# Kernel optimization log

Measured on AMD Instinct MI355X. Metric: run time of the kernel, lower is better.

The kernel has to match this reference:

```python
import jax, jax.numpy as jnp
import numpy as np

B, T, C = 4, 2048, 1024
H, DH = 16, 64  # num_heads, head_size; H*DH == C


def setup_inputs() -> dict:
    key = jax.random.key(0)
    ks = jax.random.split(key, 6)
    s = C ** -0.5  # mimic nn.Linear default init scale roughly
    x = jax.random.normal(ks[0], (B, T, C), dtype=jnp.float32)
    Wq = jax.random.normal(ks[1], (H, C, DH), dtype=jnp.float32) * s
    Wk = jax.random.normal(ks[2], (H, C, DH), dtype=jnp.float32) * s
    Wv = jax.random.normal(ks[3], (H, C, DH), dtype=jnp.float32) * s
    Wo = jax.random.normal(ks[4], (C, C), dtype=jnp.float32) * s
    bo = jax.random.normal(ks[5], (C,), dtype=jnp.float32) * s
    return {"x": x, "Wq": Wq, "Wk": Wk, "Wv": Wv, "Wo": Wo, "bo": bo}


def reference(x, Wq, Wk, Wv, Wo, bo):
    # per-head projections (no bias, as in nanoGPT Head)
    q = jnp.einsum('btc,hcd->bhtd', x, Wq)
    k = jnp.einsum('btc,hcd->bhtd', x, Wk)
    v = jnp.einsum('btc,hcd->bhtd', x, Wv)
    scale = DH ** -0.5
    scores = jnp.einsum('bhtd,bhsd->bhts', q, k) * scale  # [B,H,T,T]
    causal = jnp.tril(jnp.ones((T, T), dtype=bool))
    scores = jnp.where(causal, scores, jnp.float32(-jnp.inf))
    attn = jax.nn.softmax(scores, axis=-1)
    out = jnp.einsum('bhts,bhsd->bhtd', attn, v)  # [B,H,T,DH]
    out = out.transpose(0, 2, 1, 3).reshape(B, T, C)  # concat heads
    return out @ Wo.T + bo  # output projection (dropout=0.0 -> identity)
```

## Files before the change

kernel.cpp:

```cpp
#include <hip/hip_runtime.h>
#include <hip/hip_bf16.h>

constexpr int kB = 4, kT = 2048, kC = 1024, kH = 16, kD = 64;

typedef __attribute__((ext_vector_type(8))) short bf16x8;
typedef __attribute__((ext_vector_type(4))) short bf16x4;
typedef __attribute__((ext_vector_type(4))) float f32x4;
typedef unsigned short u16;

__device__ inline u16 f2b(float f) {
    __bf16 h = (__bf16)f;
    return __builtin_bit_cast(u16, h);
}

__device__ __forceinline__ void gl_lds16(const u16* g, u16* l) {
    __builtin_amdgcn_global_load_lds(
        (__attribute__((address_space(1))) const void*)g,
        (__attribute__((address_space(3))) void*)l, 16, 0, 0);
}

__global__ __launch_bounds__(256) void prep_kernel(const float* __restrict__ xf,
                                                   u16* __restrict__ xb,
                                                   const float* __restrict__ Wq,
                                                   const float* __restrict__ Wk,
                                                   const float* __restrict__ Wv,
                                                   u16* __restrict__ Wt) {
    __shared__ u16 tile[64][66];
    if (blockIdx.x < 8192) {
        int i = (blockIdx.x * 256 + threadIdx.x) * 4;
        float4 v = *(const float4*)(xf + i);
        ushort4 o;
        o.x = f2b(v.x); o.y = f2b(v.y); o.z = f2b(v.z); o.w = f2b(v.w);
        *(ushort4*)(xb + i) = o;
        return;
    }
    int blk = blockIdx.x - 8192;
    int ct = blk & 15;
    int h  = (blk >> 4) & 15;
    int which = blk >> 8;
    const float* W = (which == 0) ? Wq : (which == 1) ? Wk : Wv;
    const float* src = W + ((size_t)h * kC + ct * 64) * kD;
    int tid = threadIdx.x;
    int dr = (tid & 15) * 4;
    int cr = tid >> 4;
    #pragma unroll
    for (int pass = 0; pass < 4; pass++) {
        int c = pass * 16 + cr;
        float4 v = *(const float4*)(src + (size_t)c * kD + dr);
        tile[c][dr + 0] = f2b(v.x);
        tile[c][dr + 1] = f2b(v.y);
        tile[c][dr + 2] = f2b(v.z);
        tile[c][dr + 3] = f2b(v.w);
    }
    __syncthreads();
    u16* dst = Wt + ((size_t)(which * kH + h) * kD) * kC + ct * 64;
    int c4 = (tid & 15) * 4;
    int d0 = tid >> 4;
    #pragma unroll
    for (int pass = 0; pass < 4; pass++) {
        int d = pass * 16 + d0;
        ushort4 pk;
        pk.x = tile[c4 + 0][d];
        pk.y = tile[c4 + 1][d];
        pk.z = tile[c4 + 2][d];
        pk.w = tile[c4 + 3][d];
        *(ushort4*)(dst + (size_t)d * kC + c4) = pk;
    }
}

__global__ __launch_bounds__(256) void qkv_kernel(const u16* __restrict__ x,
                                                  const u16* __restrict__ Wt,
                                                  u16* __restrict__ q,
                                                  u16* __restrict__ k,
                                                  u16* __restrict__ vT) {
    __shared__ u16 Ash[128 * 32];
    __shared__ u16 Bsh[128 * 32];
    const int tid = threadIdx.x;
    const int lane = tid & 63;
    const int w = tid >> 6;
    const int mblk = blockIdx.x & 63;
    const int nblk = blockIdx.x >> 6;
    const int m0 = mblk * 128, n0 = nblk * 128;
    const int wm = (w >> 1) * 64, wn = (w & 1) * 64;
    const int col = lane & 15, quad = lane >> 4;

    const int rowa = tid >> 2;
    const int kc = (tid & 3) * 8;
    const u16* gA = x + (size_t)(m0 + rowa) * kC + kc;
    const u16* gB = Wt + (size_t)(n0 + rowa) * kC + kc;
    u16* lA = Ash + tid * 8;
    u16* lB = Bsh + tid * 8;

    f32x4 z = {0.f, 0.f, 0.f, 0.f};
    f32x4 acc[4][4];
    #pragma unroll
    for (int mi = 0; mi < 4; mi++)
        #pragma unroll
        for (int ni = 0; ni < 4; ni++) acc[mi][ni] = z;

    for (int k0 = 0; k0 < kC; k0 += 32) {
        __syncthreads();
        gl_lds16(gA + k0, lA);
        gl_lds16(gA + (size_t)64 * kC + k0, lA + 64 * 32);
        gl_lds16(gB + k0, lB);
        gl_lds16(gB + (size_t)64 * kC + k0, lB + 64 * 32);
        __syncthreads();
        bf16x8 a[4], b[4];
        #pragma unroll
        for (int mi = 0; mi < 4; mi++)
            a[mi] = *(const bf16x8*)&Ash[(wm + mi * 16 + col) * 32 + quad * 8];
        #pragma unroll
        for (int ni = 0; ni < 4; ni++)
            b[ni] = *(const bf16x8*)&Bsh[(wn + ni * 16 + col) * 32 + quad * 8];
        #pragma unroll
        for (int mi = 0; mi < 4; mi++)
            #pragma unroll
            for (int ni = 0; ni < 4; ni++)
                acc[mi][ni] = __builtin_amdgcn_mfma_f32_16x16x32_bf16(a[mi], b[ni], acc[mi][ni], 0, 0, 0);
    }

    const int nq = n0 + wn;
    const int which = nq >> 10;
    const int h = (nq & 1023) >> 6;
    const int mq = m0 + wm;
    const int b_ = mq >> 11;
    const int tq = mq & 2047;
    if (which < 2) {
        const float qs = (which == 0) ? 0.1803368801111204f : 1.0f;
        u16* base = ((which == 0) ? q : k) + ((size_t)(b_ * kH + h) * kT) * kD;
        #pragma unroll
        for (int mi = 0; mi < 4; mi++)
            #pragma unroll
            for (int ni = 0; ni < 4; ni++)
                #pragma unroll
                for (int r = 0; r < 4; r++) {
                    int t = tq + mi * 16 + quad * 4 + r;
                    base[(size_t)t * kD + ni * 16 + col] = f2b(acc[mi][ni][r] * qs);
                }
    } else {
        u16* base = vT + ((size_t)(b_ * kH + h) * kD) * kT;
        #pragma unroll
        for (int mi = 0; mi < 4; mi++)
            #pragma unroll
            for (int ni = 0; ni < 4; ni++) {
                int d = ni * 16 + col;
                int t = tq + mi * 16 + quad * 4;
                ushort4 pk;
                pk.x = f2b(acc[mi][ni][0]);
                pk.y = f2b(acc[mi][ni][1]);
                pk.z = f2b(acc[mi][ni][2]);
                pk.w = f2b(acc[mi][ni][3]);
                *(ushort4*)(base + (size_t)d * kT + t) = pk;
            }
    }
}

__device__ __forceinline__ void attn_step(const bf16x8 (&ka)[2][2],
                                          const bf16x4 (&va)[2][4],
                                          const bf16x8 (&qa)[2][2],
                                          f32x4 (&o)[2][4],
                                          float (&l_)[2],
                                          bool needmask,
                                          int s0, int t0, int col, int quad) {
    f32x4 z = {0.f, 0.f, 0.f, 0.f};
    f32x4 st[2][2];
    #pragma unroll
    for (int si = 0; si < 2; si++)
        #pragma unroll
        for (int mi = 0; mi < 2; mi++) {
            f32x4 a = __builtin_amdgcn_mfma_f32_16x16x32_bf16(ka[si][0], qa[mi][0], z, 0, 0, 0);
            st[si][mi] = __builtin_amdgcn_mfma_f32_16x16x32_bf16(ka[si][1], qa[mi][1], a, 0, 0, 0);
        }
    bf16x4 pb[2][2];
    #pragma unroll
    for (int mi = 0; mi < 2; mi++)
        #pragma unroll
        for (int si = 0; si < 2; si++) {
            bf16x4 pk;
            #pragma unroll
            for (int r = 0; r < 4; r++) {
                float p = __builtin_amdgcn_exp2f(st[si][mi][r]);
                if (needmask) {
                    int sg = s0 + si * 16 + quad * 4 + r;
                    int tg = t0 + mi * 16 + col;
                    if (sg > tg) p = 0.f;
                }
                l_[mi] += p;
                pk[r] = (short)f2b(p);
            }
            pb[mi][si] = pk;
        }
    #pragma unroll
    for (int si = 0; si < 2; si++)
        #pragma unroll
        for (int dt = 0; dt < 4; dt++)
            #pragma unroll
            for (int mi = 0; mi < 2; mi++)
                o[mi][dt] = __builtin_amdgcn_mfma_f32_16x16x16bf16_1k(va[si][dt], pb[mi][si], o[mi][dt], 0, 0, 0);
}

__global__ __launch_bounds__(256) void attn_kernel(const u16* __restrict__ q,
                                                   const u16* __restrict__ kmat,
                                                   const u16* __restrict__ vT,
                                                   u16* __restrict__ att,
                                                   const float* __restrict__ Wo,
                                                   u16* __restrict__ Wob) {
    __shared__ u16 Ksh[3][2048];
    __shared__ u16 Vsh[3][2048];
    if (blockIdx.x >= 512) {
        int i = ((blockIdx.x - 512) * 256 + threadIdx.x) * 4;
        float4 v = *(const float4*)(Wo + i);
        ushort4 o;
        o.x = f2b(v.x); o.y = f2b(v.y); o.z = f2b(v.z); o.w = f2b(v.w);
        *(ushort4*)(Wob + i) = o;
        return;
    }
    const int tid = threadIdx.x;
    const int lane = tid & 63;
    const int w = tid >> 6;
    const int bh = blockIdx.x & 63;
    const int p8 = blockIdx.x >> 6;
    const int p = p8 * 4 + w;
    const int t0a = p * 32;
    const int t0b = (63 - p) * 32;
    const int L = 63 - p8 * 4;
    const int col = lane & 15, quad = lane >> 4;

    const u16* qbase = q + (size_t)bh * kT * kD;
    const u16* kbase = kmat + (size_t)bh * kT * kD;
    const u16* vbase = vT + (size_t)bh * kD * kT;

    const int krow = tid >> 3, kpos = tid & 7;
    const u16* gK = kbase + (size_t)krow * kD + ((kpos ^ (krow & 7)) * 8);
    const int vrow = tid >> 2, vpos = tid & 3;
    const u16* gV = vbase + (size_t)vrow * kT + ((vpos ^ ((vrow >> 1) & 3)) * 8);

    bf16x8 qa[2][2][2];
    #pragma unroll
    for (int tile = 0; tile < 2; tile++) {
        int t0 = tile ? t0b : t0a;
        #pragma unroll
        for (int mi = 0; mi < 2; mi++)
            #pragma unroll
            for (int c2 = 0; c2 < 2; c2++)
                qa[tile][mi][c2] = *(const bf16x8*)(qbase + (size_t)(t0 + mi * 16 + col) * kD + c2 * 32 + quad * 8);
    }

    f32x4 z = {0.f, 0.f, 0.f, 0.f};
    f32x4 oA[2][4], oB[2][4];
    #pragma unroll
    for (int mi = 0; mi < 2; mi++)
        #pragma unroll
        for (int dt = 0; dt < 4; dt++) { oA[mi][dt] = z; oB[mi][dt] = z; }
    float lA[2] = {0.f, 0.f}, lB[2] = {0.f, 0.f};

    auto stage = [&](int buf, int tile) {
        gl_lds16(gK + (size_t)(tile * 32) * kD, &Ksh[buf][tid * 8]);
        gl_lds16(gV + tile * 32, &Vsh[buf][tid * 8]);
    };

    auto body = [&](int tile, int buf) {
        const int s0 = tile * 32;
        bf16x8 ka[2][2];
        #pragma unroll
        for (int si = 0; si < 2; si++) {
            int row = si * 16 + col;
            #pragma unroll
            for (int c2 = 0; c2 < 2; c2++)
                ka[si][c2] = *(const bf16x8*)&Ksh[buf][row * 64 + (((c2 * 4 + quad) ^ (row & 7)) * 8)];
        }
        bf16x4 va[2][4];
        #pragma unroll
        for (int si = 0; si < 2; si++)
            #pragma unroll
            for (int dt = 0; dt < 4; dt++) {
                int row = dt * 16 + col;
                int sb = si * 2 + (quad >> 1);
                va[si][dt] = *(const bf16x4*)&Vsh[buf][row * 32 + ((sb ^ ((row >> 1) & 3)) * 8) + (quad & 1) * 4];
            }
        if (s0 <= t0b)
            attn_step(ka, va, qa[1], oB, lB, s0 == t0b, s0, t0b, col, quad);
        if (s0 <= t0a)
            attn_step(ka, va, qa[0], oA, lA, s0 == t0a, s0, t0a, col, quad);
    };

    stage(0, 0);
    if (L >= 1) stage(1, 1);
    int i = 0;
    for (; i + 2 <= L; i++) {
        asm volatile("s_barrier" ::: "memory");
        stage((i + 2) % 3, i + 2);
        asm volatile("s_waitcnt vmcnt(4)" ::: "memory");
        body(i, i % 3);
    }
    if (L >= 1) {
        asm volatile("s_barrier" ::: "memory");
        asm volatile("s_waitcnt vmcnt(2)" ::: "memory");
        body(L - 1, (L - 1) % 3);
    }
    asm volatile("s_barrier" ::: "memory");
    asm volatile("s_waitcnt vmcnt(0)" ::: "memory");
    body(L, L % 3);

    #pragma unroll
    for (int mi = 0; mi < 2; mi++) {
        lA[mi] += __shfl_xor(lA[mi], 16, 64);
        lA[mi] += __shfl_xor(lA[mi], 32, 64);
        lB[mi] += __shfl_xor(lB[mi], 16, 64);
        lB[mi] += __shfl_xor(lB[mi], 32, 64);
    }

    const int b = bh / kH, hh = bh % kH;
    #pragma unroll
    for (int tile = 0; tile < 2; tile++) {
        int t0 = tile ? t0b : t0a;
        #pragma unroll
        for (int mi = 0; mi < 2; mi++) {
            float inv = 1.0f / (tile ? lB[mi] : lA[mi]);
            int t = t0 + mi * 16 + col;
            #pragma unroll
            for (int dt = 0; dt < 4; dt++) {
                f32x4 s = tile ? oB[mi][dt] : oA[mi][dt];
                ushort4 pk;
                pk.x = f2b(s[0] * inv);
                pk.y = f2b(s[1] * inv);
                pk.z = f2b(s[2] * inv);
                pk.w = f2b(s[3] * inv);
                *(ushort4*)(att + ((size_t)b * kT + t) * kC + hh * kD + dt * 16 + quad * 4) = pk;
            }
        }
    }
}

__global__ __launch_bounds__(256) void oproj_kernel(const u16* __restrict__ att,
                                                    const u16* __restrict__ Wo,
                                                    const float* __restrict__ bo,
                                                    float* __restrict__ out) {
    __shared__ u16 Ash[128 * 32];
    __shared__ u16 Bsh[128 * 32];
    const int tid = threadIdx.x;
    const int lane = tid & 63;
    const int w = tid >> 6;
    const int mblk = blockIdx.x & 63;
    const int nblk = blockIdx.x >> 6;
    const int m0 = mblk * 128, n0 = nblk * 128;
    const int wm = (w >> 1) * 64, wn = (w & 1) * 64;
    const int col = lane & 15, quad = lane >> 4;

    const int rowa = tid >> 2;
    const int kc = (tid & 3) * 8;
    const u16* gA = att + (size_t)(m0 + rowa) * kC + kc;
    const u16* gB = Wo + (size_t)(n0 + rowa) * kC + kc;
    u16* lA = Ash + tid * 8;
    u16* lB = Bsh + tid * 8;

    f32x4 z = {0.f, 0.f, 0.f, 0.f};
    f32x4 acc[4][4];
    #pragma unroll
    for (int mi = 0; mi < 4; mi++)
        #pragma unroll
        for (int ni = 0; ni < 4; ni++) acc[mi][ni] = z;

    for (int k0 = 0; k0 < kC; k0 += 32) {
        __syncthreads();
        gl_lds16(gA + k0, lA);
        gl_lds16(gA + (size_t)64 * kC + k0, lA + 64 * 32);
        gl_lds16(gB + k0, lB);
        gl_lds16(gB + (size_t)64 * kC + k0, lB + 64 * 32);
        __syncthreads();
        bf16x8 a[4], b[4];
        #pragma unroll
        for (int mi = 0; mi < 4; mi++)
            a[mi] = *(const bf16x8*)&Ash[(wm + mi * 16 + col) * 32 + quad * 8];
        #pragma unroll
        for (int ni = 0; ni < 4; ni++)
            b[ni] = *(const bf16x8*)&Bsh[(wn + ni * 16 + col) * 32 + quad * 8];
        #pragma unroll
        for (int mi = 0; mi < 4; mi++)
            #pragma unroll
            for (int ni = 0; ni < 4; ni++)
                acc[mi][ni] = __builtin_amdgcn_mfma_f32_16x16x32_bf16(a[mi], b[ni], acc[mi][ni], 0, 0, 0);
    }

    float bias[4];
    #pragma unroll
    for (int ni = 0; ni < 4; ni++) bias[ni] = bo[n0 + wn + ni * 16 + col];

    #pragma unroll
    for (int mi = 0; mi < 4; mi++)
        #pragma unroll
        for (int ni = 0; ni < 4; ni++)
            #pragma unroll
            for (int r = 0; r < 4; r++) {
                int m = m0 + wm + mi * 16 + quad * 4 + r;
                out[(size_t)m * kC + n0 + wn + ni * 16 + col] = acc[mi][ni][r] + bias[ni];
            }
}

extern "C" void kernel_launch(void* const* d_in, const int* in_sizes, int n_in,
                              void* d_out, int out_size, void* d_ws, size_t ws_size,
                              hipStream_t stream) {
    const float* x  = (const float*)d_in[0];
    const float* Wq = (const float*)d_in[1];
    const float* Wk = (const float*)d_in[2];
    const float* Wv = (const float*)d_in[3];
    const float* Wo = (const float*)d_in[4];
    const float* bo = (const float*)d_in[5];
    float* out = (float*)d_out;

    char* ws = (char*)d_ws;
    u16* Wt  = (u16*)ws;
    u16* xb  = Wt + (size_t)3 * kH * kD * kC;
    u16* qb  = xb + (size_t)kB * kT * kC;
    u16* kb  = qb + (size_t)kB * kH * kT * kD;
    u16* vTb = kb + (size_t)kB * kH * kT * kD;
    u16* att = xb;
    u16* Wob = Wt;

    prep_kernel<<<dim3(8192 + 768), dim3(256), 0, stream>>>(x, xb, Wq, Wk, Wv, Wt);
    qkv_kernel<<<dim3(1536), dim3(256), 0, stream>>>(xb, Wt, qb, kb, vTb);
    attn_kernel<<<dim3(512 + 1024), dim3(256), 0, stream>>>(qb, kb, vTb, att, Wo, Wob);
    oproj_kernel<<<dim3(512), dim3(256), 0, stream>>>(att, Wob, bo, out);
}
```

Measured before the change: 254.1 us.

## Split attention KV loop across two wave groups with LDS reduction

Doubles the attention block to 512 threads. Each half of the block processes half of the key/value tiles for the same query rows, using its own triple-buffered LDS staging area. The partial outputs and row sums are then combined through an LDS scratch reduction before normalization and store. The aim is to shorten the serial KV loop per block and raise occupancy and parallelism. The cost is extra LDS traffic, more barriers, and a larger shared-memory footprint per block.

```diff
diff --git a/kernel.cpp b/kernel.cpp
--- a/kernel.cpp
+++ b/kernel.cpp
@@ -199,16 +199,15 @@
                 o[mi][dt] = __builtin_amdgcn_mfma_f32_16x16x16bf16_1k(va[si][dt], pb[mi][si], o[mi][dt], 0, 0, 0);
 }
 
-__global__ __launch_bounds__(256) void attn_kernel(const u16* __restrict__ q,
+__global__ __launch_bounds__(512) void attn_kernel(const u16* __restrict__ q,
                                                    const u16* __restrict__ kmat,
                                                    const u16* __restrict__ vT,
                                                    u16* __restrict__ att,
                                                    const float* __restrict__ Wo,
                                                    u16* __restrict__ Wob) {
-    __shared__ u16 Ksh[3][2048];
-    __shared__ u16 Vsh[3][2048];
+    __shared__ u16 shmem[24576];
     if (blockIdx.x >= 512) {
-        int i = ((blockIdx.x - 512) * 256 + threadIdx.x) * 4;
+        int i = ((blockIdx.x - 512) * 512 + threadIdx.x) * 4;
         float4 v = *(const float4*)(Wo + i);
         ushort4 o;
         o.x = f2b(v.x); o.y = f2b(v.y); o.z = f2b(v.z); o.w = f2b(v.w);
@@ -218,22 +217,28 @@
     const int tid = threadIdx.x;
     const int lane = tid & 63;
     const int w = tid >> 6;
+    const int half = w >> 2;
     const int bh = blockIdx.x & 63;
     const int p8 = blockIdx.x >> 6;
-    const int p = p8 * 4 + w;
+    const int p = p8 * 4 + (w & 3);
     const int t0a = p * 32;
     const int t0b = (63 - p) * 32;
     const int L = 63 - p8 * 4;
+    const int n = (L + 1) / 2;
+    const int tb = half ? n : 0;
     const int col = lane & 15, quad = lane >> 4;
 
     const u16* qbase = q + (size_t)bh * kT * kD;
     const u16* kbase = kmat + (size_t)bh * kT * kD;
     const u16* vbase = vT + (size_t)bh * kD * kT;
 
-    const int krow = tid >> 3, kpos = tid & 7;
+    const int tl = tid & 255;
+    const int krow = tl >> 3, kpos = tl & 7;
     const u16* gK = kbase + (size_t)krow * kD + ((kpos ^ (krow & 7)) * 8);
-    const int vrow = tid >> 2, vpos = tid & 3;
+    const int vrow = tl >> 2, vpos = tl & 3;
     const u16* gV = vbase + (size_t)vrow * kT + ((vpos ^ ((vrow >> 1) & 3)) * 8);
+    u16* Kb0 = shmem + half * 12288;
+    u16* Vb0 = Kb0 + 6144;
 
     bf16x8 qa[2][2][2];
     #pragma unroll
@@ -255,19 +260,21 @@
     float lA[2] = {0.f, 0.f}, lB[2] = {0.f, 0.f};
 
     auto stage = [&](int buf, int tile) {
-        gl_lds16(gK + (size_t)(tile * 32) * kD, &Ksh[buf][tid * 8]);
-        gl_lds16(gV + tile * 32, &Vsh[buf][tid * 8]);
+        gl_lds16(gK + (size_t)(tile * 32) * kD, Kb0 + buf * 2048 + tl * 8);
+        gl_lds16(gV + tile * 32, Vb0 + buf * 2048 + tl * 8);
     };
 
     auto body = [&](int tile, int buf) {
         const int s0 = tile * 32;
+        const u16* Kb = Kb0 + buf * 2048;
+        const u16* Vb = Vb0 + buf * 2048;
         bf16x8 ka[2][2];
         #pragma unroll
         for (int si = 0; si < 2; si++) {
             int row = si * 16 + col;
             #pragma unroll
             for (int c2 = 0; c2 < 2; c2++)
-                ka[si][c2] = *(const bf16x8*)&Ksh[buf][row * 64 + (((c2 * 4 + quad) ^ (row & 7)) * 8)];
+                ka[si][c2] = *(const bf16x8*)&Kb[row * 64 + (((c2 * 4 + quad) ^ (row & 7)) * 8)];
         }
         bf16x4 va[2][4];
         #pragma unroll
@@ -276,7 +283,7 @@
             for (int dt = 0; dt < 4; dt++) {
                 int row = dt * 16 + col;
                 int sb = si * 2 + (quad >> 1);
-                va[si][dt] = *(const bf16x4*)&Vsh[buf][row * 32 + ((sb ^ ((row >> 1) & 3)) * 8) + (quad & 1) * 4];
+                va[si][dt] = *(const bf16x4*)&Vb[row * 32 + ((sb ^ ((row >> 1) & 3)) * 8) + (quad & 1) * 4];
             }
         if (s0 <= t0b)
             attn_step(ka, va, qa[1], oB, lB, s0 == t0b, s0, t0b, col, quad);
@@ -284,23 +291,20 @@
             attn_step(ka, va, qa[0], oA, lA, s0 == t0a, s0, t0a, col, quad);
     };
 
-    stage(0, 0);
-    if (L >= 1) stage(1, 1);
-    int i = 0;
-    for (; i + 2 <= L; i++) {
+    stage(0, tb + 0);
+    stage(1, tb + 1);
+    for (int j = 0; j + 2 <= n - 1; j++) {
         asm volatile("s_barrier" ::: "memory");
-        stage((i + 2) % 3, i + 2);
+        stage((j + 2) % 3, tb + j + 2);
         asm volatile("s_waitcnt vmcnt(4)" ::: "memory");
-        body(i, i % 3);
-    }
-    if (L >= 1) {
-        asm volatile("s_barrier" ::: "memory");
-        asm volatile("s_waitcnt vmcnt(2)" ::: "memory");
-        body(L - 1, (L - 1) % 3);
-    }
+        body(tb + j, j % 3);
+    }
+    asm volatile("s_barrier" ::: "memory");
+    asm volatile("s_waitcnt vmcnt(2)" ::: "memory");
+    body(tb + n - 2, (n - 2) % 3);
     asm volatile("s_barrier" ::: "memory");
     asm volatile("s_waitcnt vmcnt(0)" ::: "memory");
-    body(L, L % 3);
+    body(tb + n - 1, (n - 1) % 3);
 
     #pragma unroll
     for (int mi = 0; mi < 2; mi++) {
@@ -310,22 +314,79 @@
         lB[mi] += __shfl_xor(lB[mi], 32, 64);
     }
 
+    float* scr = (float*)shmem;
+    const int slot = ((w & 3) * 64 + lane) * 35;
     const int b = bh / kH, hh = bh % kH;
-    #pragma unroll
-    for (int tile = 0; tile < 2; tile++) {
-        int t0 = tile ? t0b : t0a;
+
+    __syncthreads();
+    if (half == 1) {
+        #pragma unroll
+        for (int mi = 0; mi < 2; mi++)
+            #pragma unroll
+            for (int dt = 0; dt < 4; dt++)
+                #pragma unroll
+                for (int r = 0; r < 4; r++)
+                    scr[slot + (mi * 4 + dt) * 4 + r] = oA[mi][dt][r];
+        scr[slot + 32] = lA[0];
+        scr[slot + 33] = lA[1];
+    }
+    __syncthreads();
+    if (half == 0) {
         #pragma unroll
         for (int mi = 0; mi < 2; mi++) {
-            float inv = 1.0f / (tile ? lB[mi] : lA[mi]);
-            int t = t0 + mi * 16 + col;
+            #pragma unroll
+            for (int dt = 0; dt < 4; dt++)
+                #pragma unroll
+                for (int r = 0; r < 4; r++)
+                    oA[mi][dt][r] += scr[slot + (mi * 4 + dt) * 4 + r];
+            lA[mi] += scr[slot + 32 + mi];
+        }
+        #pragma unroll
+        for (int mi = 0; mi < 2; mi++) {
+            float inv = 1.0f / lA[mi];
+            int t = t0a + mi * 16 + col;
             #pragma unroll
             for (int dt = 0; dt < 4; dt++) {
-                f32x4 s = tile ? oB[mi][dt] : oA[mi][dt];
                 ushort4 pk;
-                pk.x = f2b(s[0] * inv);
-                pk.y = f2b(s[1] * inv);
-                pk.z = f2b(s[2] * inv);
-                pk.w = f2b(s[3] * inv);
+                pk.x = f2b(oA[mi][dt][0] * inv);
+                pk.y = f2b(oA[mi][dt][1] * inv);
+                pk.z = f2b(oA[mi][dt][2] * inv);
+                pk.w = f2b(oA[mi][dt][3] * inv);
+                *(ushort4*)(att + ((size_t)b * kT + t) * kC + hh * kD + dt * 16 + quad * 4) = pk;
+            }
+        }
+        #pragma unroll
+        for (int mi = 0; mi < 2; mi++)
+            #pragma unroll
+            for (int dt = 0; dt < 4; dt++)
+                #pragma unroll
+                for (int r = 0; r < 4; r++)
+                    scr[slot + (mi * 4 + dt) * 4 + r] = oB[mi][dt][r];
+        scr[slot + 32] = lB[0];
+        scr[slot + 33] = lB[1];
+    }
+    __syncthreads();
+    if (half == 1) {
+        #pragma unroll
+        for (int mi = 0; mi < 2; mi++) {
+            #pragma unroll
+            for (int dt = 0; dt < 4; dt++)
+                #pragma unroll
+                for (int r = 0; r < 4; r++)
+                    oB[mi][dt][r] += scr[slot + (mi * 4 + dt) * 4 + r];
+            lB[mi] += scr[slot + 32 + mi];
+        }
+        #pragma unroll
+        for (int mi = 0; mi < 2; mi++) {
+            float inv = 1.0f / lB[mi];
+            int t = t0b + mi * 16 + col;
+            #pragma unroll
+            for (int dt = 0; dt < 4; dt++) {
+                ushort4 pk;
+                pk.x = f2b(oB[mi][dt][0] * inv);
+                pk.y = f2b(oB[mi][dt][1] * inv);
+                pk.z = f2b(oB[mi][dt][2] * inv);
+                pk.w = f2b(oB[mi][dt][3] * inv);
                 *(ushort4*)(att + ((size_t)b * kT + t) * kC + hh * kD + dt * 16 + quad * 4) = pk;
             }
         }
@@ -419,6 +480,6 @@
 
     prep_kernel<<<dim3(8192 + 768), dim3(256), 0, stream>>>(x, xb, Wq, Wk, Wv, Wt);
     qkv_kernel<<<dim3(1536), dim3(256), 0, stream>>>(xb, Wt, qb, kb, vTb);
-    attn_kernel<<<dim3(512 + 1024), dim3(256), 0, stream>>>(qb, kb, vTb, att, Wo, Wob);
+    attn_kernel<<<dim3(512 + 512), dim3(512), 0, stream>>>(qb, kb, vTb, att, Wo, Wob);
     oproj_kernel<<<dim3(512), dim3(256), 0, stream>>>(att, Wob, bo, out);
 }
```

After: 254.7 us. No clear change (+0.2%).

## Give each wave private double-buffered K/V LDS staging and drop block barriers

Applied to the files above, without the earlier changes.

Replaces the block-shared triple-buffered K/V staging with per-wave double buffers, so each wave loads its own K/V tiles and iterates only up to its own causal limit. This removes the s_barrier calls and the extra tiles that shorter-range waves used to wait on. The cost is four times more global-to-LDS traffic for the same K/V tiles, since each wave loads them independently, plus a larger LDS footprint (64KB) that may lower occupancy.

```diff
diff --git a/kernel.cpp b/kernel.cpp
--- a/kernel.cpp
+++ b/kernel.cpp
@@ -205,8 +205,7 @@
                                                    u16* __restrict__ att,
                                                    const float* __restrict__ Wo,
                                                    u16* __restrict__ Wob) {
-    __shared__ u16 Ksh[3][2048];
-    __shared__ u16 Vsh[3][2048];
+    __shared__ u16 shmem[4][2][4096];
     if (blockIdx.x >= 512) {
         int i = ((blockIdx.x - 512) * 256 + threadIdx.x) * 4;
         float4 v = *(const float4*)(Wo + i);
@@ -223,17 +222,15 @@
     const int p = p8 * 4 + w;
     const int t0a = p * 32;
     const int t0b = (63 - p) * 32;
-    const int L = 63 - p8 * 4;
+    const int Lw = 63 - p8 * 4 - w;
     const int col = lane & 15, quad = lane >> 4;
 
     const u16* qbase = q + (size_t)bh * kT * kD;
     const u16* kbase = kmat + (size_t)bh * kT * kD;
     const u16* vbase = vT + (size_t)bh * kD * kT;
 
-    const int krow = tid >> 3, kpos = tid & 7;
-    const u16* gK = kbase + (size_t)krow * kD + ((kpos ^ (krow & 7)) * 8);
-    const int vrow = tid >> 2, vpos = tid & 3;
-    const u16* gV = vbase + (size_t)vrow * kT + ((vpos ^ ((vrow >> 1) & 3)) * 8);
+    const u16* gK0 = kbase + (size_t)(lane >> 3) * kD + (((lane & 7) ^ (lane >> 3)) * 8);
+    const u16* gV0 = vbase + (size_t)(lane >> 2) * kT + (((lane & 3) ^ ((lane >> 3) & 3)) * 8);
 
     bf16x8 qa[2][2][2];
     #pragma unroll
@@ -245,6 +242,7 @@
             for (int c2 = 0; c2 < 2; c2++)
                 qa[tile][mi][c2] = *(const bf16x8*)(qbase + (size_t)(t0 + mi * 16 + col) * kD + c2 * 32 + quad * 8);
     }
+    asm volatile("s_waitcnt vmcnt(0)" ::: "memory");
 
     f32x4 z = {0.f, 0.f, 0.f, 0.f};
     f32x4 oA[2][4], oB[2][4];
@@ -255,19 +253,32 @@
     float lA[2] = {0.f, 0.f}, lB[2] = {0.f, 0.f};
 
     auto stage = [&](int buf, int tile) {
-        gl_lds16(gK + (size_t)(tile * 32) * kD, &Ksh[buf][tid * 8]);
-        gl_lds16(gV + tile * 32, &Vsh[buf][tid * 8]);
+        u16* Kd = &shmem[w][buf][0] + lane * 8;
+        u16* Vd = &shmem[w][buf][2048] + lane * 8;
+        const u16* gk = gK0 + (size_t)(tile * 32) * kD;
+        const u16* gv = gV0 + tile * 32;
+        #pragma unroll
+        for (int i = 0; i < 4; i++) {
+            gl_lds16(gk + (size_t)(i * 8) * kD, Kd + i * 512);
+            gl_lds16(gv + (size_t)(i * 16) * kT, Vd + i * 512);
+        }
     };
 
-    auto body = [&](int tile, int buf) {
-        const int s0 = tile * 32;
+    stage(0, 0);
+    if (Lw >= 1) stage(1, 1);
+    for (int j = 0; j <= Lw; j++) {
+        if (j < Lw) { asm volatile("s_waitcnt vmcnt(8)" ::: "memory"); }
+        else        { asm volatile("s_waitcnt vmcnt(0)" ::: "memory"); }
+        const int buf = j & 1;
+        const u16* Kb = &shmem[w][buf][0];
+        const u16* Vb = Kb + 2048;
         bf16x8 ka[2][2];
         #pragma unroll
         for (int si = 0; si < 2; si++) {
             int row = si * 16 + col;
             #pragma unroll
             for (int c2 = 0; c2 < 2; c2++)
-                ka[si][c2] = *(const bf16x8*)&Ksh[buf][row * 64 + (((c2 * 4 + quad) ^ (row & 7)) * 8)];
+                ka[si][c2] = *(const bf16x8*)&Kb[row * 64 + (((c2 * 4 + quad) ^ (row & 7)) * 8)];
         }
         bf16x4 va[2][4];
         #pragma unroll
@@ -276,31 +287,15 @@
             for (int dt = 0; dt < 4; dt++) {
                 int row = dt * 16 + col;
                 int sb = si * 2 + (quad >> 1);
-                va[si][dt] = *(const bf16x4*)&Vsh[buf][row * 32 + ((sb ^ ((row >> 1) & 3)) * 8) + (quad & 1) * 4];
+                va[si][dt] = *(const bf16x4*)&Vb[row * 32 + ((sb ^ ((row >> 1) & 3)) * 8) + (quad & 1) * 4];
             }
-        if (s0 <= t0b)
-            attn_step(ka, va, qa[1], oB, lB, s0 == t0b, s0, t0b, col, quad);
-        if (s0 <= t0a)
-            attn_step(ka, va, qa[0], oA, lA, s0 == t0a, s0, t0a, col, quad);
-    };
-
-    stage(0, 0);
-    if (L >= 1) stage(1, 1);
-    int i = 0;
-    for (; i + 2 <= L; i++) {
-        asm volatile("s_barrier" ::: "memory");
-        stage((i + 2) % 3, i + 2);
-        asm volatile("s_waitcnt vmcnt(4)" ::: "memory");
-        body(i, i % 3);
-    }
-    if (L >= 1) {
-        asm volatile("s_barrier" ::: "memory");
-        asm volatile("s_waitcnt vmcnt(2)" ::: "memory");
-        body(L - 1, (L - 1) % 3);
-    }
-    asm volatile("s_barrier" ::: "memory");
-    asm volatile("s_waitcnt vmcnt(0)" ::: "memory");
-    body(L, L % 3);
+        asm volatile("s_waitcnt lgkmcnt(0)" ::: "memory");
+        if (j + 2 <= Lw) stage(buf, j + 2);
+        const int s0 = j * 32;
+        attn_step(ka, va, qa[1], oB, lB, j == Lw, s0, t0b, col, quad);
+        if (j <= p)
+            attn_step(ka, va, qa[0], oA, lA, j == p, s0, t0a, col, quad);
+    }
 
     #pragma unroll
     for (int mi = 0; mi < 2; mi++) {
```

New measurement: 247.9 us. 2.4% less time.
